# Optimization experiments

Hardware: AMD Instinct MI355X
Metric: run time of the kernel (lower is better)

Reference implementation:

```python
import jax, jax.numpy as jnp
import numpy as np

N = 50000        # nodes
E = 1600000      # edges (avg degree 32)
D = 64           # emb_dim
H = 2            # heads
NEG_SLOPE = 0.2
BOND_VOCAB = 5   # vocab per bond feature (3 categorical features)


def setup_inputs() -> dict:
    key = jax.random.key(0)
    ks = jax.random.split(key, 8)
    x = jax.random.normal(ks[0], (N, D), jnp.float32)
    edge_index = jax.random.randint(ks[1], (2, E), 0, N)
    edge_attr = jax.random.randint(ks[2], (E, 3), 0, BOND_VOCAB)
    W = jax.random.normal(ks[3], (D, H * D), jnp.float32) / np.float32(np.sqrt(D))
    b_W = jnp.zeros((H * D,), jnp.float32)
    att = jax.random.normal(ks[4], (1, H, 2 * D), jnp.float32) * 0.1
    bias = jnp.zeros((D,), jnp.float32)
    bond_emb = jax.random.normal(ks[5], (3, BOND_VOCAB, H * D), jnp.float32) * 0.1
    return dict(x=x, edge_index=edge_index, edge_attr=edge_attr,
                W=W, b_W=b_W, att=att, bias=bias, bond_emb=bond_emb)


def reference(x, edge_index, edge_attr, W, b_W, att, bias, bond_emb):
    row, col = edge_index[0], edge_index[1]  # src (x_j), dst (x_i / aggregation target)
    # BondEncoder: sum of per-feature categorical embeddings -> [E, H*D]
    e = (bond_emb[0][edge_attr[:, 0]]
         + bond_emb[1][edge_attr[:, 1]]
         + bond_emb[2][edge_attr[:, 2]])
    h = x @ W + b_W                                   # [N, H*D]
    x_j = h[row].reshape(-1, H, D) + e.reshape(-1, H, D)   # message source + edge emb
    x_i = h[col].reshape(-1, H, D)                         # message target
    # attention logits: [E, H]
    alpha = (jnp.concatenate([x_i, x_j], axis=-1) * att).sum(-1)
    alpha = jnp.where(alpha >= 0, alpha, NEG_SLOPE * alpha)  # leaky_relu
    # segment softmax over edge_index[0] (source node), PyG semantics
    m = jax.ops.segment_max(alpha, row, num_segments=N)      # [N, H]
    m = jnp.where(jnp.isfinite(m), m, 0.0)                   # empty segments -> 0
    ea = jnp.exp(alpha - m[row])
    s = jax.ops.segment_sum(ea, row, num_segments=N)
    alpha = ea / (s[row] + 1e-16)
    # weighted messages, scatter-add to destination nodes
    msg = x_j * alpha[:, :, None]                            # [E, H, D]
    aggr = jax.ops.segment_sum(msg, col, num_segments=N)     # [N, H, D]
    # update: mean over heads + bias
    return aggr.mean(axis=1) + bias
```

## Files before the change

kernel.cpp:

```cpp
#include <hip/hip_runtime.h>
#include <hip/hip_bf16.h>
#include <math.h>

#define NEG_SLOPE 0.2f
#define CHUNK 2048
#define NPB2 128
#define SCAP 5120

__device__ __forceinline__ unsigned f2bf(float f) {
  unsigned u = __float_as_uint(f);
  return (u + 0x7fffu + ((u >> 16) & 1u)) >> 16;
}

__global__ __launch_bounds__(256) void k1_gemm(
    const float* __restrict__ x, const float* __restrict__ W,
    const float* __restrict__ bW, const float* __restrict__ att,
    unsigned int* __restrict__ hb, float* __restrict__ ai,
    float* __restrict__ aj, int Nn) {
  int t = threadIdx.x;
  int lane = t & 63;
  int wid = blockIdx.x * (blockDim.x >> 6) + (t >> 6);
  int nwaves = gridDim.x * (blockDim.x >> 6);

  float Wr0[64], Wr1[64];
#pragma unroll
  for (int k = 0; k < 64; ++k) {
    Wr0[k] = W[k * 128 + lane];
    Wr1[k] = W[k * 128 + 64 + lane];
  }
  float bs0 = bW[lane], bs1 = bW[64 + lane];
  float ati0 = att[lane];
  float atj0 = att[64 + lane];
  float ati1 = att[128 + lane];
  float atj1 = att[192 + lane];

  for (int row = wid; row < Nn; row += nwaves) {
    int r = __builtin_amdgcn_readfirstlane(row);
    const float* __restrict__ xr = x + (size_t)r * 64;
    float a0a = 0.f, a0b = 0.f, a1a = 0.f, a1b = 0.f;
#pragma unroll
    for (int k = 0; k < 64; k += 2) {
      float xk0 = xr[k], xk1 = xr[k + 1];
      a0a = fmaf(xk0, Wr0[k], a0a);
      a1a = fmaf(xk0, Wr1[k], a1a);
      a0b = fmaf(xk1, Wr0[k + 1], a0b);
      a1b = fmaf(xk1, Wr1[k + 1], a1b);
    }
    float h0 = a0a + a0b + bs0;
    float h1 = a1a + a1b + bs1;
    hb[(size_t)r * 64 + lane] = f2bf(h0) | (f2bf(h1) << 16);

    float ti0 = ati0 * h0, tj0 = atj0 * h0;
    float ti1 = ati1 * h1, tj1 = atj1 * h1;
    ti0 += __shfl_xor(ti0, 32, 64);
    tj0 += __shfl_xor(tj0, 32, 64);
    ti1 += __shfl_xor(ti1, 32, 64);
    tj1 += __shfl_xor(tj1, 32, 64);
    float mi = (lane < 32) ? ti0 : ti1;
    float mj = (lane < 32) ? tj0 : tj1;
#pragma unroll
    for (int off = 16; off > 0; off >>= 1) {
      mi += __shfl_xor(mi, off, 64);
      mj += __shfl_xor(mj, off, 64);
    }
    if ((lane & 31) == 0) {
      ai[r * 2 + (lane >> 5)] = mi;
      aj[r * 2 + (lane >> 5)] = mj;
    }
  }
}

__global__ __launch_bounds__(256) void k_bin(
    const int* __restrict__ ei, const int* __restrict__ eattr,
    unsigned int* __restrict__ rec, int* __restrict__ cnt_tbl,
    int* __restrict__ base_tbl, unsigned int* __restrict__ rec_src,
    int* __restrict__ cnt_tbl2, int* __restrict__ base_tbl2, int Ee, int NCB) {
  __shared__ unsigned sbuf[CHUNK];
  __shared__ unsigned sbuf2[CHUNK];
  __shared__ int hist[512], cur[512], hist2[512], cur2[512];
  __shared__ int ssc[256];
  int t = threadIdx.x;
  for (int i = t; i < NCB; i += 256) { hist[i] = 0; hist2[i] = 0; }
  __syncthreads();
  int start = blockIdx.x * CHUNK;
  int end = min(start + CHUNK, Ee);
  int cnt = end - start;
  int cbv[CHUNK / 256], cb2v[CHUNK / 256];
  unsigned pkv[CHUNK / 256], pk2v[CHUNK / 256];
  int nk = 0;
  for (int e = start + t; e < end; e += 256, ++nk) {
    int dst = __builtin_nontemporal_load(&ei[Ee + e]);
    int src = __builtin_nontemporal_load(&ei[e]);
    int a0 = __builtin_nontemporal_load(&eattr[e * 3]);
    int a1 = __builtin_nontemporal_load(&eattr[e * 3 + 1]);
    int a2 = __builtin_nontemporal_load(&eattr[e * 3 + 2]);
    unsigned c012 = (unsigned)(a0 + 5 * a1 + 25 * a2);
    cbv[nk] = dst >> 7;
    pkv[nk] = (unsigned)src | (c012 << 16) | ((unsigned)(dst & 127) << 23);
    cb2v[nk] = src >> 7;
    pk2v[nk] = (unsigned)dst | ((unsigned)(src & 127) << 17) | (c012 << 24);
    atomicAdd(&hist[dst >> 7], 1);
    atomicAdd(&hist2[src >> 7], 1);
  }
  __syncthreads();
  {
    int per = (NCB + 255) / 256;
    int loc[4];
    int lsum = 0;
#pragma unroll 2
    for (int j = 0; j < per; ++j) {
      int idx = t * per + j;
      int v = (idx < NCB) ? hist[idx] : 0;
      loc[j] = lsum;
      lsum += v;
    }
    ssc[t] = lsum;
    __syncthreads();
#pragma unroll
    for (int o = 1; o < 256; o <<= 1) {
      int xv = (t >= o) ? ssc[t - o] : 0;
      __syncthreads();
      ssc[t] += xv;
      __syncthreads();
    }
    int excl = ssc[t] - lsum;
#pragma unroll 2
    for (int j = 0; j < per; ++j) {
      int idx = t * per + j;
      if (idx < NCB) cur[idx] = excl + loc[j];
    }
    __syncthreads();
    lsum = 0;
#pragma unroll 2
    for (int j = 0; j < per; ++j) {
      int idx = t * per + j;
      int v = (idx < NCB) ? hist2[idx] : 0;
      loc[j] = lsum;
      lsum += v;
    }
    ssc[t] = lsum;
    __syncthreads();
#pragma unroll
    for (int o = 1; o < 256; o <<= 1) {
      int xv = (t >= o) ? ssc[t - o] : 0;
      __syncthreads();
      ssc[t] += xv;
      __syncthreads();
    }
    excl = ssc[t] - lsum;
#pragma unroll 2
    for (int j = 0; j < per; ++j) {
      int idx = t * per + j;
      if (idx < NCB) cur2[idx] = excl + loc[j];
    }
  }
  __syncthreads();
  for (int i = t; i < NCB; i += 256) {
    cnt_tbl[blockIdx.x * NCB + i] = hist[i];
    base_tbl[blockIdx.x * NCB + i] = cur[i];
    cnt_tbl2[blockIdx.x * NCB + i] = hist2[i];
    base_tbl2[blockIdx.x * NCB + i] = cur2[i];
  }
  __syncthreads();
  for (int k = 0; k < nk; ++k) {
    int pos = atomicAdd(&cur[cbv[k]], 1);
    sbuf[pos] = pkv[k];
    int pos2 = atomicAdd(&cur2[cb2v[k]], 1);
    sbuf2[pos2] = pk2v[k];
  }
  __syncthreads();
  for (int i = t; i < cnt; i += 256) {
    __builtin_nontemporal_store(sbuf[i], &rec[start + i]);
    __builtin_nontemporal_store(sbuf2[i], &rec_src[start + i]);
  }
}

__global__ __launch_bounds__(256) void k_segoff_ab(
    const int* __restrict__ cnt_tbl, int* __restrict__ segdst,
    int* __restrict__ btot, const int* __restrict__ cnt_tbl2,
    int* __restrict__ segdst2, int* __restrict__ btot2, int NCB, int NBLK) {
  __shared__ int s[256];
  int t = threadIdx.x;
  int bid = blockIdx.x;
  const int* __restrict__ ct = (bid < NCB) ? cnt_tbl : cnt_tbl2;
  int* __restrict__ sd = (bid < NCB) ? segdst : segdst2;
  int* __restrict__ bt = (bid < NCB) ? btot : btot2;
  int cb = (bid < NCB) ? bid : bid - NCB;
  int per = (NBLK + 255) / 256;
  int loc[8];
  int sum = 0;
  for (int j = 0; j < per; ++j) {
    int blk = t * per + j;
    int v = (blk < NBLK) ? ct[blk * NCB + cb] : 0;
    loc[j] = sum;
    sum += v;
  }
  s[t] = sum;
  __syncthreads();
#pragma unroll
  for (int o = 1; o < 256; o <<= 1) {
    int xv = (t >= o) ? s[t - o] : 0;
    __syncthreads();
    s[t] += xv;
    __syncthreads();
  }
  int excl = s[t] - sum;
  for (int j = 0; j < per; ++j) {
    int blk = t * per + j;
    if (blk < NBLK) sd[cb * NBLK + blk] = excl + loc[j];
  }
  if (t == 255) bt[cb] = s[255];
}

__global__ __launch_bounds__(512) void k_segoff_b(
    const int* __restrict__ btot, int* __restrict__ coarse_base, int NCB, int Ee) {
  __shared__ int s[512];
  int t = threadIdx.x;
  int v = (t < NCB) ? btot[t] : 0;
  s[t] = v;
  __syncthreads();
#pragma unroll
  for (int o = 1; o < 512; o <<= 1) {
    int xv = (t >= o) ? s[t - o] : 0;
    __syncthreads();
    s[t] += xv;
    __syncthreads();
  }
  if (t < NCB) coarse_base[t] = s[t] - v;
  if (t == 0) coarse_base[NCB] = Ee;
}

__global__ __launch_bounds__(256) void k_sacc(
    const unsigned int* __restrict__ rec_src, const int* __restrict__ cnt_tbl2,
    const int* __restrict__ base_tbl2, const int* __restrict__ segdst2,
    const int* __restrict__ btot2, const float2* __restrict__ ai2,
    const float2* __restrict__ aj2, const float* __restrict__ att,
    const float* __restrict__ bemb, float* __restrict__ sden,
    int Nn, int NCB, int NBLK) {
  __shared__ unsigned ubuf[SCAP];
  __shared__ float sdl[NPB2 * 2];
  __shared__ float2 ajs[NPB2];
  __shared__ float tbl[30];
  int t = threadIdx.x;
  int cb = blockIdx.x;
  if (t < 30) {
    int f = t / 10, rem = t % 10, c = rem >> 1, hh = rem & 1;
    float sacc = 0.f;
    for (int d = 0; d < 64; ++d)
      sacc += att[hh * 128 + 64 + d] * bemb[(f * 5 + c) * 128 + hh * 64 + d];
    tbl[t] = sacc;
  }
  int node0 = cb << 7;
  if (t < NPB2 && node0 + t < Nn) ajs[t] = aj2[node0 + t];
  sdl[t] = 0.f;
  int total = btot2[cb];
  __syncthreads();
  bool fits = (total <= SCAP);

#define SACC_BODY(U, AIV)                                                      \
  {                                                                            \
    int sl = ((U) >> 17) & 127;                                                \
    int c012 = ((U) >> 24) & 127;                                              \
    int a0 = c012 % 5, a1 = (c012 / 5) % 5, a2 = c012 / 25;                    \
    float2 ajv = ajs[sl];                                                      \
    float lg0 = AIV.x + ajv.x + tbl[a0 * 2] + tbl[10 + a1 * 2] +               \
                tbl[20 + a2 * 2];                                              \
    float lg1 = AIV.y + ajv.y + tbl[a0 * 2 + 1] + tbl[10 + a1 * 2 + 1] +       \
                tbl[20 + a2 * 2 + 1];                                          \
    lg0 = lg0 >= 0.f ? lg0 : NEG_SLOPE * lg0;                                  \
    lg1 = lg1 >= 0.f ? lg1 : NEG_SLOPE * lg1;                                  \
    atomicAdd(&sdl[sl * 2], __expf(lg0));                                      \
    atomicAdd(&sdl[sl * 2 + 1], __expf(lg1));                                  \
  }

  if (fits) {
    for (int blk = t; blk < NBLK; blk += 256) {
      int len = cnt_tbl2[blk * NCB + cb];
      if (!len) continue;
      int sp = blk * CHUNK + base_tbl2[blk * NCB + cb];
      int dp = segdst2[cb * NBLK + blk];
      for (int j = 0; j < len; ++j) ubuf[dp + j] = rec_src[sp + j];
    }
    __syncthreads();
    int i = t;
    for (; i + 7 * 256 < total; i += 8 * 256) {
      unsigned u[8];
      float2 aiv[8];
#pragma unroll
      for (int k = 0; k < 8; ++k) u[k] = ubuf[i + k * 256];
#pragma unroll
      for (int k = 0; k < 8; ++k) aiv[k] = ai2[u[k] & 0x1FFFF];
#pragma unroll
      for (int k = 0; k < 8; ++k) SACC_BODY(u[k], aiv[k])
    }
    for (; i < total; i += 256) {
      unsigned u = ubuf[i];
      float2 aiv = ai2[u & 0x1FFFF];
      SACC_BODY(u, aiv)
    }
  } else {
    for (int blk = t; blk < NBLK; blk += 256) {
      int len = cnt_tbl2[blk * NCB + cb];
      int sp = blk * CHUNK + base_tbl2[blk * NCB + cb];
      for (int j = 0; j < len; ++j) {
        unsigned u = rec_src[sp + j];
        float2 aiv = ai2[u & 0x1FFFF];
        SACC_BODY(u, aiv)
      }
    }
  }
#undef SACC_BODY
  __syncthreads();
  if (node0 + (t >> 1) < Nn) sden[(size_t)node0 * 2 + t] = sdl[t];
}

__global__ __launch_bounds__(256) void k_sort(
    const unsigned int* __restrict__ rec, const int* __restrict__ cnt_tbl,
    const int* __restrict__ base_tbl, const int* __restrict__ segdst,
    const int* __restrict__ coarse_base, const float2* __restrict__ ai2,
    const float2* __restrict__ aj2, const float2* __restrict__ sd2,
    const float* __restrict__ att, const float* __restrict__ bemb,
    unsigned int* __restrict__ eix2, float2* __restrict__ alpha2,
    int* __restrict__ off, int Nn, int NCB, int NBLK, int Ee) {
  __shared__ unsigned ubuf[SCAP];
  __shared__ unsigned ubuf2[SCAP];
  __shared__ int hist[NPB2], basex[NPB2], curx[NPB2];
  __shared__ float tbl[30];
  __shared__ float2 ais[NPB2];
  int t = threadIdx.x;
  int cb = blockIdx.x;
  if (t < 30) {
    int f = t / 10, rem = t % 10, c = rem >> 1, hh = rem & 1;
    float sacc = 0.f;
    for (int d = 0; d < 64; ++d)
      sacc += att[hh * 128 + 64 + d] * bemb[(f * 5 + c) * 128 + hh * 64 + d];
    tbl[t] = sacc;
  }
  int node0 = cb << 7;
  if (t < NPB2) {
    hist[t] = 0;
    if (node0 + t < Nn) ais[t] = ai2[node0 + t];
  }
  int gbase = coarse_base[cb];
  int total = coarse_base[cb + 1] - gbase;
  __syncthreads();
  bool fits = (total <= SCAP);

  if (fits) {
    for (int blk = t; blk < NBLK; blk += 256) {
      int len = cnt_tbl[blk * NCB + cb];
      if (!len) continue;
      int sp = blk * CHUNK + base_tbl[blk * NCB + cb];
      int dp = segdst[cb * NBLK + blk];
      for (int j = 0; j < len; ++j) ubuf[dp + j] = rec[sp + j];
    }
    __syncthreads();
    for (int i = t; i < total; i += 256)
      atomicAdd(&hist[(ubuf[i] >> 23) & 127], 1);
    __syncthreads();
    if (t == 0) {
      int s = 0;
      for (int i = 0; i < NPB2; ++i) { basex[i] = s; s += hist[i]; }
    }
    __syncthreads();
    if (t < NPB2) {
      curx[t] = basex[t];
      if (node0 + t < Nn) off[node0 + t] = gbase + basex[t];
    }
    if (cb == 0 && t == 0) off[Nn] = Ee;
    __syncthreads();
    for (int i = t; i < total; i += 256) {
      unsigned u = ubuf[i];
      int pos = atomicAdd(&curx[(u >> 23) & 127], 1);
      ubuf2[pos] = u;
    }
    __syncthreads();

#define OUT_BODY(I, U, AJV, SDV)                                               \
    {                                                                          \
      int src = (U) & 0xFFFF;                                                  \
      int c012 = ((U) >> 16) & 127;                                            \
      int dl = ((U) >> 23) & 127;                                              \
      int a0 = c012 % 5, a1 = (c012 / 5) % 5, a2 = c012 / 25;                  \
      float2 aiv = ais[dl];                                                    \
      float lg0 = aiv.x + AJV.x + tbl[a0 * 2] + tbl[10 + a1 * 2] +             \
                  tbl[20 + a2 * 2];                                            \
      float lg1 = aiv.y + AJV.y + tbl[a0 * 2 + 1] + tbl[10 + a1 * 2 + 1] +     \
                  tbl[20 + a2 * 2 + 1];                                        \
      lg0 = lg0 >= 0.f ? lg0 : NEG_SLOPE * lg0;                                \
      lg1 = lg1 >= 0.f ? lg1 : NEG_SLOPE * lg1;                                \
      eix2[gbase + (I)] = (unsigned)src | ((unsigned)a0 << 16) |               \
                          ((unsigned)a1 << 19) | ((unsigned)a2 << 22);         \
      alpha2[gbase + (I)] = make_float2(__expf(lg0) / (SDV.x + 1e-16f),        \
                                        __expf(lg1) / (SDV.y + 1e-16f));       \
    }

    int i = t;
    for (; i + 3 * 256 < total; i += 4 * 256) {
      unsigned u[4];
      float2 ajv[4], sdv[4];
#pragma unroll
      for (int k = 0; k < 4; ++k) u[k] = ubuf2[i + k * 256];
#pragma unroll
      for (int k = 0; k < 4; ++k) ajv[k] = aj2[u[k] & 0xFFFF];
#pragma unroll
      for (int k = 0; k < 4; ++k) sdv[k] = sd2[u[k] & 0xFFFF];
#pragma unroll
      for (int k = 0; k < 4; ++k) OUT_BODY(i + k * 256, u[k], ajv[k], sdv[k])
    }
    for (; i < total; i += 256) {
      unsigned u = ubuf2[i];
      float2 ajv = aj2[u & 0xFFFF];
      float2 sdv = sd2[u & 0xFFFF];
      OUT_BODY(i, u, ajv, sdv)
    }
#undef OUT_BODY
  } else {
    for (int blk = t; blk < NBLK; blk += 256) {
      int len = cnt_tbl[blk * NCB + cb];
      int sp = blk * CHUNK + base_tbl[blk * NCB + cb];
      for (int j = 0; j < len; ++j)
        atomicAdd(&hist[(rec[sp + j] >> 23) & 127], 1);
    }
    __syncthreads();
    if (t == 0) {
      int s = 0;
      for (int i = 0; i < NPB2; ++i) { basex[i] = s; s += hist[i]; }
    }
    __syncthreads();
    if (t < NPB2) {
      curx[t] = basex[t];
      if (node0 + t < Nn) off[node0 + t] = gbase + basex[t];
    }
    if (cb == 0 && t == 0) off[Nn] = Ee;
    __syncthreads();
    for (int blk = t; blk < NBLK; blk += 256) {
      int len = cnt_tbl[blk * NCB + cb];
      int sp = blk * CHUNK + base_tbl[blk * NCB + cb];
      for (int j = 0; j < len; ++j) {
        unsigned u = rec[sp + j];
        int src = u & 0xFFFF;
        int c012 = (u >> 16) & 127;
        int dl = (u >> 23) & 127;
        int a0 = c012 % 5, a1 = (c012 / 5) % 5, a2 = c012 / 25;
        float2 aiv = ais[dl];
        float2 ajv = aj2[src];
        float2 sdv = sd2[src];
        float lg0 = aiv.x + ajv.x + tbl[a0 * 2] + tbl[10 + a1 * 2] + tbl[20 + a2 * 2];
        float lg1 = aiv.y + ajv.y + tbl[a0 * 2 + 1] + tbl[10 + a1 * 2 + 1] +
                    tbl[20 + a2 * 2 + 1];
        lg0 = lg0 >= 0.f ? lg0 : NEG_SLOPE * lg0;
        lg1 = lg1 >= 0.f ? lg1 : NEG_SLOPE * lg1;
        int pos = gbase + atomicAdd(&curx[dl], 1);
        eix2[pos] = (unsigned)src | ((unsigned)a0 << 16) | ((unsigned)a1 << 19) |
                    ((unsigned)a2 << 22);
        alpha2[pos] = make_float2(__expf(lg0) / (sdv.x + 1e-16f),
                                  __expf(lg1) / (sdv.y + 1e-16f));
      }
    }
  }
}

__global__ __launch_bounds__(256) void k_gather(
    const unsigned int* __restrict__ eix, const float2* __restrict__ alpha2,
    const int* __restrict__ off, const unsigned int* __restrict__ hb,
    const float* __restrict__ bemb, const float* __restrict__ bias,
    float* __restrict__ out, int Nn) {
  __shared__ float bembs[15 * 128];
  __shared__ float wsm[4][32];
  int t = threadIdx.x;
  for (int i = t; i < 15 * 128; i += 256) bembs[i] = bemb[i];
  __syncthreads();
  int wave = t >> 6, lane = t & 63;
  int n = blockIdx.x * 4 + wave;
  if (n >= Nn) return;
  int p0 = __builtin_amdgcn_readfirstlane(off[n]);
  int p1 = __builtin_amdgcn_readfirstlane(off[n + 1]);
  int myf = lane / 5;
  int myc = lane % 5;
  bool active = lane < 15;
  int myshift = 16 + 3 * myf;
  int mycEff = active ? myc : 8;
  float w0 = 0.f, w1 = 0.f;
  float acc0 = 0.f, acc1 = 0.f;

#define EDGE_BODY(U, HV, AL)                                                   \
  {                                                                            \
    acc0 = fmaf(AL.x, __uint_as_float((HV) << 16), acc0);                      \
    acc1 = fmaf(AL.y, __uint_as_float((HV) & 0xffff0000u), acc1);              \
    int sel = (int)(((U) >> myshift) & 7u);                                    \
    float m = (sel == mycEff) ? 1.0f : 0.0f;                                   \
    w0 = fmaf(m, AL.x, w0);                                                    \
    w1 = fmaf(m, AL.y, w1);                                                    \
  }

  int p = p0;
  for (; p + 8 <= p1; p += 8) {
    unsigned u[8], hv[8];
    float2 al[8];
#pragma unroll
    for (int k = 0; k < 8; ++k) u[k] = eix[p + k];
#pragma unroll
    for (int k = 0; k < 8; ++k) al[k] = alpha2[p + k];
#pragma unroll
    for (int k = 0; k < 8; ++k) {
      const unsigned* __restrict__ hrow = hb + ((size_t)(u[k] & 0xFFFFu) << 6);
      hv[k] = hrow[lane];
    }
#pragma unroll
    for (int k = 0; k < 8; ++k) EDGE_BODY(u[k], hv[k], al[k])
  }
  for (; p < p1; ++p) {
    unsigned u0 = eix[p];
    float2 al0 = alpha2[p];
    const unsigned* __restrict__ hrow = hb + ((size_t)(u0 & 0xFFFFu) << 6);
    unsigned hv0 = hrow[lane];
    EDGE_BODY(u0, hv0, al0)
  }
#undef EDGE_BODY

  if (active) {
    wsm[wave][lane * 2] = w0;
    wsm[wave][lane * 2 + 1] = w1;
  }
#pragma unroll
  for (int k = 0; k < 15; ++k) {
    acc0 += wsm[wave][k * 2] * bembs[k * 128 + lane];
    acc1 += wsm[wave][k * 2 + 1] * bembs[k * 128 + 64 + lane];
  }
  out[(size_t)n * 64 + lane] = 0.5f * (acc0 + acc1) + bias[lane];
}

extern "C" void kernel_launch(void* const* d_in, const int* in_sizes, int n_in,
                              void* d_out, int out_size, void* d_ws, size_t ws_size,
                              hipStream_t stream) {
  const float* x    = (const float*)d_in[0];
  const int*   ei   = (const int*)d_in[1];
  const int*   eatt = (const int*)d_in[2];
  const float* W    = (const float*)d_in[3];
  const float* bW   = (const float*)d_in[4];
  const float* att  = (const float*)d_in[5];
  const float* bias = (const float*)d_in[6];
  const float* bemb = (const float*)d_in[7];
  int Nn = in_sizes[0] / 64;
  int Ee = in_sizes[1] / 2;
  int NCB = (Nn + NPB2 - 1) / NPB2;
  int NBLK = (Ee + CHUNK - 1) / CHUNK;

  char* ws = (char*)d_ws;
  ws = (char*)(((uintptr_t)ws + 15) & ~(uintptr_t)15);
  float* aj = (float*)ws;                 ws += (size_t)Nn * 2 * 4;
  float* sden = (float*)ws;               ws += (size_t)Nn * 2 * 4;
  float* ai = (float*)ws;                 ws += (size_t)Nn * 2 * 4;
  unsigned int* hb = (unsigned int*)ws;   ws += (size_t)Nn * 64 * 4;
  unsigned int* rec = (unsigned int*)ws;  ws += (size_t)NBLK * CHUNK * 4;
  unsigned int* rec_src = (unsigned int*)ws; ws += (size_t)NBLK * CHUNK * 4;
  unsigned int* eix2 = (unsigned int*)ws; ws += (size_t)Ee * 4;
  float2* alpha2 = (float2*)ws;           ws += (size_t)Ee * 8;
  int* off = (int*)ws;                    ws += (size_t)(Nn + 1) * 4;
  int* cnt_tbl = (int*)ws;                ws += (size_t)NBLK * NCB * 4;
  int* base_tbl = (int*)ws;               ws += (size_t)NBLK * NCB * 4;
  int* cnt_tbl2 = (int*)ws;               ws += (size_t)NBLK * NCB * 4;
  int* base_tbl2 = (int*)ws;              ws += (size_t)NBLK * NCB * 4;
  int* segdst = (int*)ws;                 ws += (size_t)NCB * NBLK * 4;
  int* segdst2 = (int*)ws;                ws += (size_t)NCB * NBLK * 4;
  int* coarse_base = (int*)ws;            ws += (size_t)(NCB + 1) * 4;
  int* btot = (int*)ws;                   ws += (size_t)NCB * 4;
  int* btot2 = (int*)ws;                  ws += (size_t)NCB * 4;

  k1_gemm<<<1024, 256, 0, stream>>>(x, W, bW, att, hb, ai, aj, Nn);
  k_bin<<<NBLK, 256, 0, stream>>>(ei, eatt, rec, cnt_tbl, base_tbl, rec_src,
                                  cnt_tbl2, base_tbl2, Ee, NCB);
  k_segoff_ab<<<2 * NCB, 256, 0, stream>>>(cnt_tbl, segdst, btot, cnt_tbl2,
                                           segdst2, btot2, NCB, NBLK);
  k_segoff_b<<<1, 512, 0, stream>>>(btot, coarse_base, NCB, Ee);
  k_sacc<<<NCB, 256, 0, stream>>>(rec_src, cnt_tbl2, base_tbl2, segdst2, btot2,
                                  (const float2*)ai, (const float2*)aj, att,
                                  bemb, sden, Nn, NCB, NBLK);
  k_sort<<<NCB, 256, 0, stream>>>(rec, cnt_tbl, base_tbl, segdst, coarse_base,
                                  (const float2*)ai, (const float2*)aj,
                                  (const float2*)sden, att, bemb, eix2, alpha2,
                                  off, Nn, NCB, NBLK, Ee);
  k_gather<<<(Nn + 3) / 4, 256, 0, stream>>>(eix2, alpha2, off, hb, bemb, bias,
                                             (float*)d_out, Nn);
}
```

Baseline: 282.5 us.

## Merge softmax-denominator and sort kernels, defer normalization to gather

The denominator-accumulation kernel and the sort/alpha kernel are merged into one launch with 2*NCB blocks. The sort half no longer depends on the denominators, so it stores the unnormalized exp and the two halves can run concurrently. The gather kernel now loads a per-source reciprocal denominator and multiplies it into each edge weight. This removes a launch and a serialization point, at the cost of an extra random per-edge load in gather and a larger shared-memory footprint per block. The sort path's inner loop is also unrolled from 4 to 8.

```diff
diff --git a/kernel.cpp b/kernel.cpp
--- a/kernel.cpp
+++ b/kernel.cpp
@@ -230,19 +230,25 @@
   if (t == 0) coarse_base[NCB] = Ee;
 }
 
-__global__ __launch_bounds__(256) void k_sacc(
+__global__ __launch_bounds__(256) void k_mid(
+    const unsigned int* __restrict__ rec, const int* __restrict__ cnt_tbl,
+    const int* __restrict__ base_tbl, const int* __restrict__ segdst,
+    const int* __restrict__ coarse_base,
     const unsigned int* __restrict__ rec_src, const int* __restrict__ cnt_tbl2,
     const int* __restrict__ base_tbl2, const int* __restrict__ segdst2,
-    const int* __restrict__ btot2, const float2* __restrict__ ai2,
-    const float2* __restrict__ aj2, const float* __restrict__ att,
-    const float* __restrict__ bemb, float* __restrict__ sden,
-    int Nn, int NCB, int NBLK) {
+    const int* __restrict__ btot2,
+    const float2* __restrict__ ai2, const float2* __restrict__ aj2,
+    const float* __restrict__ att, const float* __restrict__ bemb,
+    float* __restrict__ rden, unsigned int* __restrict__ eix2,
+    float2* __restrict__ alpha2, int* __restrict__ off,
+    int Nn, int NCB, int NBLK, int Ee) {
   __shared__ unsigned ubuf[SCAP];
+  __shared__ unsigned ubuf2[SCAP];
+  __shared__ int hist[NPB2], basex[NPB2], curx[NPB2];
+  __shared__ float tbl[30];
+  __shared__ float2 nodev[NPB2];
   __shared__ float sdl[NPB2 * 2];
-  __shared__ float2 ajs[NPB2];
-  __shared__ float tbl[30];
   int t = threadIdx.x;
-  int cb = blockIdx.x;
   if (t < 30) {
     int f = t / 10, rem = t % 10, c = rem >> 1, hh = rem & 1;
     float sacc = 0.f;
@@ -250,212 +256,191 @@
       sacc += att[hh * 128 + 64 + d] * bemb[(f * 5 + c) * 128 + hh * 64 + d];
     tbl[t] = sacc;
   }
-  int node0 = cb << 7;
-  if (t < NPB2 && node0 + t < Nn) ajs[t] = aj2[node0 + t];
-  sdl[t] = 0.f;
-  int total = btot2[cb];
-  __syncthreads();
-  bool fits = (total <= SCAP);
+
+  if (blockIdx.x < NCB) {
+    int cb = blockIdx.x;
+    int node0 = cb << 7;
+    if (t < NPB2 && node0 + t < Nn) nodev[t] = aj2[node0 + t];
+    sdl[t] = 0.f;
+    int total = btot2[cb];
+    __syncthreads();
+    bool fits = (total <= SCAP);
 
 #define SACC_BODY(U, AIV)                                                      \
-  {                                                                            \
-    int sl = ((U) >> 17) & 127;                                                \
-    int c012 = ((U) >> 24) & 127;                                              \
-    int a0 = c012 % 5, a1 = (c012 / 5) % 5, a2 = c012 / 25;                    \
-    float2 ajv = ajs[sl];                                                      \
-    float lg0 = AIV.x + ajv.x + tbl[a0 * 2] + tbl[10 + a1 * 2] +               \
-                tbl[20 + a2 * 2];                                              \
-    float lg1 = AIV.y + ajv.y + tbl[a0 * 2 + 1] + tbl[10 + a1 * 2 + 1] +       \
-                tbl[20 + a2 * 2 + 1];                                          \
-    lg0 = lg0 >= 0.f ? lg0 : NEG_SLOPE * lg0;                                  \
-    lg1 = lg1 >= 0.f ? lg1 : NEG_SLOPE * lg1;                                  \
-    atomicAdd(&sdl[sl * 2], __expf(lg0));                                      \
-    atomicAdd(&sdl[sl * 2 + 1], __expf(lg1));                                  \
-  }
-
-  if (fits) {
-    for (int blk = t; blk < NBLK; blk += 256) {
-      int len = cnt_tbl2[blk * NCB + cb];
-      if (!len) continue;
-      int sp = blk * CHUNK + base_tbl2[blk * NCB + cb];
-      int dp = segdst2[cb * NBLK + blk];
-      for (int j = 0; j < len; ++j) ubuf[dp + j] = rec_src[sp + j];
-    }
-    __syncthreads();
-    int i = t;
-    for (; i + 7 * 256 < total; i += 8 * 256) {
-      unsigned u[8];
-      float2 aiv[8];
-#pragma unroll
-      for (int k = 0; k < 8; ++k) u[k] = ubuf[i + k * 256];
-#pragma unroll
-      for (int k = 0; k < 8; ++k) aiv[k] = ai2[u[k] & 0x1FFFF];
-#pragma unroll
-      for (int k = 0; k < 8; ++k) SACC_BODY(u[k], aiv[k])
-    }
-    for (; i < total; i += 256) {
-      unsigned u = ubuf[i];
-      float2 aiv = ai2[u & 0x1FFFF];
-      SACC_BODY(u, aiv)
-    }
-  } else {
-    for (int blk = t; blk < NBLK; blk += 256) {
-      int len = cnt_tbl2[blk * NCB + cb];
-      int sp = blk * CHUNK + base_tbl2[blk * NCB + cb];
-      for (int j = 0; j < len; ++j) {
-        unsigned u = rec_src[sp + j];
-        float2 aiv = ai2[u & 0x1FFFF];
-        SACC_BODY(u, aiv)
-      }
-    }
-  }
-#undef SACC_BODY
-  __syncthreads();
-  if (node0 + (t >> 1) < Nn) sden[(size_t)node0 * 2 + t] = sdl[t];
-}
-
-__global__ __launch_bounds__(256) void k_sort(
-    const unsigned int* __restrict__ rec, const int* __restrict__ cnt_tbl,
-    const int* __restrict__ base_tbl, const int* __restrict__ segdst,
-    const int* __restrict__ coarse_base, const float2* __restrict__ ai2,
-    const float2* __restrict__ aj2, const float2* __restrict__ sd2,
-    const float* __restrict__ att, const float* __restrict__ bemb,
-    unsigned int* __restrict__ eix2, float2* __restrict__ alpha2,
-    int* __restrict__ off, int Nn, int NCB, int NBLK, int Ee) {
-  __shared__ unsigned ubuf[SCAP];
-  __shared__ unsigned ubuf2[SCAP];
-  __shared__ int hist[NPB2], basex[NPB2], curx[NPB2];
-  __shared__ float tbl[30];
-  __shared__ float2 ais[NPB2];
-  int t = threadIdx.x;
-  int cb = blockIdx.x;
-  if (t < 30) {
-    int f = t / 10, rem = t % 10, c = rem >> 1, hh = rem & 1;
-    float sacc = 0.f;
-    for (int d = 0; d < 64; ++d)
-      sacc += att[hh * 128 + 64 + d] * bemb[(f * 5 + c) * 128 + hh * 64 + d];
-    tbl[t] = sacc;
-  }
-  int node0 = cb << 7;
-  if (t < NPB2) {
-    hist[t] = 0;
-    if (node0 + t < Nn) ais[t] = ai2[node0 + t];
-  }
-  int gbase = coarse_base[cb];
-  int total = coarse_base[cb + 1] - gbase;
-  __syncthreads();
-  bool fits = (total <= SCAP);
-
-  if (fits) {
-    for (int blk = t; blk < NBLK; blk += 256) {
-      int len = cnt_tbl[blk * NCB + cb];
-      if (!len) continue;
-      int sp = blk * CHUNK + base_tbl[blk * NCB + cb];
-      int dp = segdst[cb * NBLK + blk];
-      for (int j = 0; j < len; ++j) ubuf[dp + j] = rec[sp + j];
-    }
-    __syncthreads();
-    for (int i = t; i < total; i += 256)
-      atomicAdd(&hist[(ubuf[i] >> 23) & 127], 1);
-    __syncthreads();
-    if (t == 0) {
-      int s = 0;
-      for (int i = 0; i < NPB2; ++i) { basex[i] = s; s += hist[i]; }
-    }
-    __syncthreads();
-    if (t < NPB2) {
-      curx[t] = basex[t];
-      if (node0 + t < Nn) off[node0 + t] = gbase + basex[t];
-    }
-    if (cb == 0 && t == 0) off[Nn] = Ee;
-    __syncthreads();
-    for (int i = t; i < total; i += 256) {
-      unsigned u = ubuf[i];
-      int pos = atomicAdd(&curx[(u >> 23) & 127], 1);
-      ubuf2[pos] = u;
-    }
-    __syncthreads();
-
-#define OUT_BODY(I, U, AJV, SDV)                                               \
     {                                                                          \
-      int src = (U) & 0xFFFF;                                                  \
-      int c012 = ((U) >> 16) & 127;                                            \
-      int dl = ((U) >> 23) & 127;                                              \
+      int sl = ((U) >> 17) & 127;                                              \
+      int c012 = ((U) >> 24) & 127;                                            \
       int a0 = c012 % 5, a1 = (c012 / 5) % 5, a2 = c012 / 25;                  \
-      float2 aiv = ais[dl];                                                    \
-      float lg0 = aiv.x + AJV.x + tbl[a0 * 2] + tbl[10 + a1 * 2] +             \
+      float2 ajv = nodev[sl];                                                  \
+      float lg0 = AIV.x + ajv.x + tbl[a0 * 2] + tbl[10 + a1 * 2] +             \
                   tbl[20 + a2 * 2];                                            \
-      float lg1 = aiv.y + AJV.y + tbl[a0 * 2 + 1] + tbl[10 + a1 * 2 + 1] +     \
+      float lg1 = AIV.y + ajv.y + tbl[a0 * 2 + 1] + tbl[10 + a1 * 2 + 1] +     \
                   tbl[20 + a2 * 2 + 1];                                        \
       lg0 = lg0 >= 0.f ? lg0 : NEG_SLOPE * lg0;                                \
       lg1 = lg1 >= 0.f ? lg1 : NEG_SLOPE * lg1;                                \
-      eix2[gbase + (I)] = (unsigned)src | ((unsigned)a0 << 16) |               \
-                          ((unsigned)a1 << 19) | ((unsigned)a2 << 22);         \
-      alpha2[gbase + (I)] = make_float2(__expf(lg0) / (SDV.x + 1e-16f),        \
-                                        __expf(lg1) / (SDV.y + 1e-16f));       \
-    }
-
-    int i = t;
-    for (; i + 3 * 256 < total; i += 4 * 256) {
-      unsigned u[4];
-      float2 ajv[4], sdv[4];
-#pragma unroll
-      for (int k = 0; k < 4; ++k) u[k] = ubuf2[i + k * 256];
-#pragma unroll
-      for (int k = 0; k < 4; ++k) ajv[k] = aj2[u[k] & 0xFFFF];
-#pragma unroll
-      for (int k = 0; k < 4; ++k) sdv[k] = sd2[u[k] & 0xFFFF];
-#pragma unroll
-      for (int k = 0; k < 4; ++k) OUT_BODY(i + k * 256, u[k], ajv[k], sdv[k])
-    }
-    for (; i < total; i += 256) {
-      unsigned u = ubuf2[i];
-      float2 ajv = aj2[u & 0xFFFF];
-      float2 sdv = sd2[u & 0xFFFF];
-      OUT_BODY(i, u, ajv, sdv)
-    }
+      atomicAdd(&sdl[sl * 2], __expf(lg0));                                    \
+      atomicAdd(&sdl[sl * 2 + 1], __expf(lg1));                                \
+    }
+
+    if (fits) {
+      for (int blk = t; blk < NBLK; blk += 256) {
+        int len = cnt_tbl2[blk * NCB + cb];
+        if (!len) continue;
+        int sp = blk * CHUNK + base_tbl2[blk * NCB + cb];
+        int dp = segdst2[cb * NBLK + blk];
+        for (int j = 0; j < len; ++j) ubuf[dp + j] = rec_src[sp + j];
+      }
+      __syncthreads();
+      int i = t;
+      for (; i + 7 * 256 < total; i += 8 * 256) {
+        unsigned u[8];
+        float2 aiv[8];
+#pragma unroll
+        for (int k = 0; k < 8; ++k) u[k] = ubuf[i + k * 256];
+#pragma unroll
+        for (int k = 0; k < 8; ++k) aiv[k] = ai2[u[k] & 0x1FFFF];
+#pragma unroll
+        for (int k = 0; k < 8; ++k) SACC_BODY(u[k], aiv[k])
+      }
+      for (; i < total; i += 256) {
+        unsigned u = ubuf[i];
+        float2 aiv = ai2[u & 0x1FFFF];
+        SACC_BODY(u, aiv)
+      }
+    } else {
+      for (int blk = t; blk < NBLK; blk += 256) {
+        int len = cnt_tbl2[blk * NCB + cb];
+        int sp = blk * CHUNK + base_tbl2[blk * NCB + cb];
+        for (int j = 0; j < len; ++j) {
+          unsigned u = rec_src[sp + j];
+          float2 aiv = ai2[u & 0x1FFFF];
+          SACC_BODY(u, aiv)
+        }
+      }
+    }
+#undef SACC_BODY
+    __syncthreads();
+    if (node0 + (t >> 1) < Nn)
+      rden[(size_t)node0 * 2 + t] = 1.0f / (sdl[t] + 1e-16f);
+
+  } else {
+    int cb = blockIdx.x - NCB;
+    int node0 = cb << 7;
+    if (t < NPB2) {
+      hist[t] = 0;
+      if (node0 + t < Nn) nodev[t] = ai2[node0 + t];
+    }
+    int gbase = coarse_base[cb];
+    int total = coarse_base[cb + 1] - gbase;
+    __syncthreads();
+    bool fits = (total <= SCAP);
+
+    if (fits) {
+      for (int blk = t; blk < NBLK; blk += 256) {
+        int len = cnt_tbl[blk * NCB + cb];
+        if (!len) continue;
+        int sp = blk * CHUNK + base_tbl[blk * NCB + cb];
+        int dp = segdst[cb * NBLK + blk];
+        for (int j = 0; j < len; ++j) ubuf[dp + j] = rec[sp + j];
+      }
+      __syncthreads();
+      for (int i = t; i < total; i += 256)
+        atomicAdd(&hist[(ubuf[i] >> 23) & 127], 1);
+      __syncthreads();
+      if (t == 0) {
+        int s = 0;
+        for (int i = 0; i < NPB2; ++i) { basex[i] = s; s += hist[i]; }
+      }
+      __syncthreads();
+      if (t < NPB2) {
+        curx[t] = basex[t];
+        if (node0 + t < Nn) off[node0 + t] = gbase + basex[t];
+      }
+      if (cb == 0 && t == 0) off[Nn] = Ee;
+      __syncthreads();
+      for (int i = t; i < total; i += 256) {
+        unsigned u = ubuf[i];
+        int pos = atomicAdd(&curx[(u >> 23) & 127], 1);
+        ubuf2[pos] = u;
+      }
+      __syncthreads();
+
+#define OUT_BODY(I, U, AJV)                                                    \
+      {                                                                        \
+        int src = (U) & 0xFFFF;                                                \
+        int c012 = ((U) >> 16) & 127;                                          \
+        int dl = ((U) >> 23) & 127;                                            \
+        int a0 = c012 % 5, a1 = (c012 / 5) % 5, a2 = c012 / 25;                \
+        float2 aiv = nodev[dl];                                                \
+        float lg0 = aiv.x + AJV.x + tbl[a0 * 2] + tbl[10 + a1 * 2] +           \
+                    tbl[20 + a2 * 2];                                          \
+        float lg1 = aiv.y + AJV.y + tbl[a0 * 2 + 1] + tbl[10 + a1 * 2 + 1] +   \
+                    tbl[20 + a2 * 2 + 1];                                      \
+        lg0 = lg0 >= 0.f ? lg0 : NEG_SLOPE * lg0;                              \
+        lg1 = lg1 >= 0.f ? lg1 : NEG_SLOPE * lg1;                              \
+        eix2[gbase + (I)] = (unsigned)src | ((unsigned)a0 << 16) |             \
+                            ((unsigned)a1 << 19) | ((unsigned)a2 << 22);       \
+        alpha2[gbase + (I)] = make_float2(__expf(lg0), __expf(lg1));           \
+      }
+
+      int i = t;
+      for (; i + 7 * 256 < total; i += 8 * 256) {
+        unsigned u[8];
+        float2 ajv[8];
+#pragma unroll
+        for (int k = 0; k < 8; ++k) u[k] = ubuf2[i + k * 256];
+#pragma unroll
+        for (int k = 0; k < 8; ++k) ajv[k] = aj2[u[k] & 0xFFFF];
+#pragma unroll
+        for (int k = 0; k < 8; ++k) OUT_BODY(i + k * 256, u[k], ajv[k])
+      }
+      for (; i < total; i += 256) {
+        unsigned u = ubuf2[i];
+        float2 ajv = aj2[u & 0xFFFF];
+        OUT_BODY(i, u, ajv)
+      }
 #undef OUT_BODY
-  } else {
-    for (int blk = t; blk < NBLK; blk += 256) {
-      int len = cnt_tbl[blk * NCB + cb];
-      int sp = blk * CHUNK + base_tbl[blk * NCB + cb];
-      for (int j = 0; j < len; ++j)
-        atomicAdd(&hist[(rec[sp + j] >> 23) & 127], 1);
-    }
-    __syncthreads();
-    if (t == 0) {
-      int s = 0;
-      for (int i = 0; i < NPB2; ++i) { basex[i] = s; s += hist[i]; }
-    }
-    __syncthreads();
-    if (t < NPB2) {
-      curx[t] = basex[t];
-      if (node0 + t < Nn) off[node0 + t] = gbase + basex[t];
-    }
-    if (cb == 0 && t == 0) off[Nn] = Ee;
-    __syncthreads();
-    for (int blk = t; blk < NBLK; blk += 256) {
-      int len = cnt_tbl[blk * NCB + cb];
-      int sp = blk * CHUNK + base_tbl[blk * NCB + cb];
-      for (int j = 0; j < len; ++j) {
-        unsigned u = rec[sp + j];
-        int src = u & 0xFFFF;
-        int c012 = (u >> 16) & 127;
-        int dl = (u >> 23) & 127;
-        int a0 = c012 % 5, a1 = (c012 / 5) % 5, a2 = c012 / 25;
-        float2 aiv = ais[dl];
-        float2 ajv = aj2[src];
-        float2 sdv = sd2[src];
-        float lg0 = aiv.x + ajv.x + tbl[a0 * 2] + tbl[10 + a1 * 2] + tbl[20 + a2 * 2];
-        float lg1 = aiv.y + ajv.y + tbl[a0 * 2 + 1] + tbl[10 + a1 * 2 + 1] +
-                    tbl[20 + a2 * 2 + 1];
-        lg0 = lg0 >= 0.f ? lg0 : NEG_SLOPE * lg0;
-        lg1 = lg1 >= 0.f ? lg1 : NEG_SLOPE * lg1;
-        int pos = gbase + atomicAdd(&curx[dl], 1);
-        eix2[pos] = (unsigned)src | ((unsigned)a0 << 16) | ((unsigned)a1 << 19) |
-                    ((unsigned)a2 << 22);
-        alpha2[pos] = make_float2(__expf(lg0) / (sdv.x + 1e-16f),
-                                  __expf(lg1) / (sdv.y + 1e-16f));
+    } else {
+      for (int blk = t; blk < NBLK; blk += 256) {
+        int len = cnt_tbl[blk * NCB + cb];
+        int sp = blk * CHUNK + base_tbl[blk * NCB + cb];
+        for (int j = 0; j < len; ++j)
+          atomicAdd(&hist[(rec[sp + j] >> 23) & 127], 1);
+      }
+      __syncthreads();
+      if (t == 0) {
+        int s = 0;
+        for (int i = 0; i < NPB2; ++i) { basex[i] = s; s += hist[i]; }
+      }
+      __syncthreads();
+      if (t < NPB2) {
+        curx[t] = basex[t];
+        if (node0 + t < Nn) off[node0 + t] = gbase + basex[t];
+      }
+      if (cb == 0 && t == 0) off[Nn] = Ee;
+      __syncthreads();
+      for (int blk = t; blk < NBLK; blk += 256) {
+        int len = cnt_tbl[blk * NCB + cb];
+        int sp = blk * CHUNK + base_tbl[blk * NCB + cb];
+        for (int j = 0; j < len; ++j) {
+          unsigned u = rec[sp + j];
+          int src = u & 0xFFFF;
+          int c012 = (u >> 16) & 127;
+          int dl = (u >> 23) & 127;
+          int a0 = c012 % 5, a1 = (c012 / 5) % 5, a2 = c012 / 25;
+          float2 aiv = nodev[dl];
+          float2 ajv = aj2[src];
+          float lg0 = aiv.x + ajv.x + tbl[a0 * 2] + tbl[10 + a1 * 2] +
+                      tbl[20 + a2 * 2];
+          float lg1 = aiv.y + ajv.y + tbl[a0 * 2 + 1] + tbl[10 + a1 * 2 + 1] +
+                      tbl[20 + a2 * 2 + 1];
+          lg0 = lg0 >= 0.f ? lg0 : NEG_SLOPE * lg0;
+          lg1 = lg1 >= 0.f ? lg1 : NEG_SLOPE * lg1;
+          int pos = gbase + atomicAdd(&curx[dl], 1);
+          eix2[pos] = (unsigned)src | ((unsigned)a0 << 16) |
+                      ((unsigned)a1 << 19) | ((unsigned)a2 << 22);
+          alpha2[pos] = make_float2(__expf(lg0), __expf(lg1));
+        }
       }
     }
   }
@@ -464,8 +449,8 @@
 __global__ __launch_bounds__(256) void k_gather(
     const unsigned int* __restrict__ eix, const float2* __restrict__ alpha2,
     const int* __restrict__ off, const unsigned int* __restrict__ hb,
-    const float* __restrict__ bemb, const float* __restrict__ bias,
-    float* __restrict__ out, int Nn) {
+    const float2* __restrict__ rden2, const float* __restrict__ bemb,
+    const float* __restrict__ bias, float* __restrict__ out, int Nn) {
   __shared__ float bembs[15 * 128];
   __shared__ float wsm[4][32];
   int t = threadIdx.x;
@@ -484,38 +469,42 @@
   float w0 = 0.f, w1 = 0.f;
   float acc0 = 0.f, acc1 = 0.f;
 
-#define EDGE_BODY(U, HV, AL)                                                   \
+#define EDGE_BODY(U, HV, AL, RD)                                               \
   {                                                                            \
-    acc0 = fmaf(AL.x, __uint_as_float((HV) << 16), acc0);                      \
-    acc1 = fmaf(AL.y, __uint_as_float((HV) & 0xffff0000u), acc1);              \
+    float aw0 = (AL).x * (RD).x, aw1 = (AL).y * (RD).y;                        \
+    acc0 = fmaf(aw0, __uint_as_float((HV) << 16), acc0);                       \
+    acc1 = fmaf(aw1, __uint_as_float((HV) & 0xffff0000u), acc1);               \
     int sel = (int)(((U) >> myshift) & 7u);                                    \
     float m = (sel == mycEff) ? 1.0f : 0.0f;                                   \
-    w0 = fmaf(m, AL.x, w0);                                                    \
-    w1 = fmaf(m, AL.y, w1);                                                    \
+    w0 = fmaf(m, aw0, w0);                                                     \
+    w1 = fmaf(m, aw1, w1);                                                     \
   }
 
   int p = p0;
   for (; p + 8 <= p1; p += 8) {
     unsigned u[8], hv[8];
-    float2 al[8];
+    float2 al[8], rd[8];
 #pragma unroll
     for (int k = 0; k < 8; ++k) u[k] = eix[p + k];
 #pragma unroll
     for (int k = 0; k < 8; ++k) al[k] = alpha2[p + k];
+#pragma unroll
+    for (int k = 0; k < 8; ++k) rd[k] = rden2[u[k] & 0xFFFFu];
 #pragma unroll
     for (int k = 0; k < 8; ++k) {
       const unsigned* __restrict__ hrow = hb + ((size_t)(u[k] & 0xFFFFu) << 6);
       hv[k] = hrow[lane];
     }
 #pragma unroll
-    for (int k = 0; k < 8; ++k) EDGE_BODY(u[k], hv[k], al[k])
+    for (int k = 0; k < 8; ++k) EDGE_BODY(u[k], hv[k], al[k], rd[k])
   }
   for (; p < p1; ++p) {
-    unsigned u0 = eix[p];
-    float2 al0 = alpha2[p];
-    const unsigned* __restrict__ hrow = hb + ((size_t)(u0 & 0xFFFFu) << 6);
-    unsigned hv0 = hrow[lane];
-    EDGE_BODY(u0, hv0, al0)
+    unsigned ue = eix[p];
+    float2 ale = alpha2[p];
+    float2 rde = rden2[ue & 0xFFFFu];
+    const unsigned* __restrict__ hrow = hb + ((size_t)(ue & 0xFFFFu) << 6);
+    unsigned hve = hrow[lane];
+    EDGE_BODY(ue, hve, ale, rde)
   }
 #undef EDGE_BODY
 
@@ -550,7 +539,7 @@
   char* ws = (char*)d_ws;
   ws = (char*)(((uintptr_t)ws + 15) & ~(uintptr_t)15);
   float* aj = (float*)ws;                 ws += (size_t)Nn * 2 * 4;
-  float* sden = (float*)ws;               ws += (size_t)Nn * 2 * 4;
+  float* rden = (float*)ws;               ws += (size_t)Nn * 2 * 4;
   float* ai = (float*)ws;                 ws += (size_t)Nn * 2 * 4;
   unsigned int* hb = (unsigned int*)ws;   ws += (size_t)Nn * 64 * 4;
   unsigned int* rec = (unsigned int*)ws;  ws += (size_t)NBLK * CHUNK * 4;
@@ -574,13 +563,12 @@
   k_segoff_ab<<<2 * NCB, 256, 0, stream>>>(cnt_tbl, segdst, btot, cnt_tbl2,
                                            segdst2, btot2, NCB, NBLK);
   k_segoff_b<<<1, 512, 0, stream>>>(btot, coarse_base, NCB, Ee);
-  k_sacc<<<NCB, 256, 0, stream>>>(rec_src, cnt_tbl2, base_tbl2, segdst2, btot2,
-                                  (const float2*)ai, (const float2*)aj, att,
-                                  bemb, sden, Nn, NCB, NBLK);
-  k_sort<<<NCB, 256, 0, stream>>>(rec, cnt_tbl, base_tbl, segdst, coarse_base,
-                                  (const float2*)ai, (const float2*)aj,
-                                  (const float2*)sden, att, bemb, eix2, alpha2,
-                                  off, Nn, NCB, NBLK, Ee);
-  k_gather<<<(Nn + 3) / 4, 256, 0, stream>>>(eix2, alpha2, off, hb, bemb, bias,
+  k_mid<<<2 * NCB, 256, 0, stream>>>(rec, cnt_tbl, base_tbl, segdst,
+                                     coarse_base, rec_src, cnt_tbl2, base_tbl2,
+                                     segdst2, btot2, (const float2*)ai,
+                                     (const float2*)aj, att, bemb, rden, eix2,
+                                     alpha2, off, Nn, NCB, NBLK, Ee);
+  k_gather<<<(Nn + 3) / 4, 256, 0, stream>>>(eix2, alpha2, off, hb,
+                                             (const float2*)rden, bemb, bias,
                                              (float*)d_out, Nn);
 }
```

Result: no change. 281.2 us (-0.5%).
